# Optimization experiments

Hardware: AMD Instinct MI355X
Metric: run time of the kernel (lower is better)

The kernel has to match this reference:

```python
import jax, jax.numpy as jnp
import numpy as np

EPS_SINK = 0.05
MAX_ITER = 50
THRESH = 0.1
LN_EPS = 1e-5


def _nu_from_score_map(score_map):
    # score_map: [B, K, H, W] -> nu: [B, K]
    B, K, H, W = score_map.shape
    pred = jnp.argmax(score_map, axis=1).reshape(B, H * W)      # [B, HW]
    one_hot = jax.nn.one_hot(pred, K, dtype=score_map.dtype)     # [B, HW, K]
    counts = one_hot.sum(axis=1)                                 # [B, K]
    nu = counts / (counts.sum(axis=1, keepdims=True) + 1e-8)
    nu = nu + 1e-6
    return nu / nu.sum(axis=1, keepdims=True)


def _sinkhorn(x, y, nu):
    # x: [B, N, C], y: [B, M, C], nu: [B, M]
    B, N, _ = x.shape
    M = y.shape[1]
    xn = x / jnp.linalg.norm(x, axis=2, keepdims=True)
    yn = y / jnp.linalg.norm(y, axis=2, keepdims=True)
    cost = 1.0 - jnp.einsum('bnc,bmc->bnm', xn, yn)              # [B, N, M]
    Kmat = jnp.exp(-cost / EPS_SINK)
    mu = jnp.full((B, N), 1.0 / N, dtype=x.dtype)
    u0 = jnp.zeros((B, N), dtype=x.dtype)
    v0 = jnp.zeros((B, M), dtype=x.dtype)

    def step(carry, _):
        u, v, done = carry
        u_new = mu / (jnp.einsum('bnm,bm->bn', Kmat, v) + 1e-8)
        v_new = nu / (jnp.einsum('bnm,bn->bm', Kmat, u_new) + 1e-8)
        err = jnp.abs(u_new - u).sum(-1).mean()
        # torch breaks AFTER the update, so the breaking iteration's u,v are kept;
        # 'done' freezes subsequent iterations (early-stop semantics).
        u_out = jnp.where(done, u, u_new)
        v_out = jnp.where(done, v, v_new)
        return (u_out, v_out, done | (err < THRESH)), None

    (u, v, _), _ = jax.lax.scan(step, (u0, v0, jnp.array(False)), None, length=MAX_ITER)
    pi = u[:, :, None] * Kmat * v[:, None, :]                    # [B, N, M]
    ot_cost = jnp.sum(pi * cost, axis=(1, 2))                    # [B] (reduction='none')
    return ot_cost, pi


def _layernorm(x, gamma, beta):
    mean = x.mean(-1, keepdims=True)
    var = ((x - mean) ** 2).mean(-1, keepdims=True)
    return (x - mean) * jax.lax.rsqrt(var + LN_EPS) * gamma + beta


def setup_inputs() -> dict:
    key = jax.random.key(0)
    k1, k2, k3, k4 = jax.random.split(key, 4)
    B, HW, C, K, H, W = 16, 4096, 512, 32, 64, 64
    return {
        'source_feat': jax.random.normal(k1, (B, HW, C), jnp.float32),
        'target_feat_matrix': jax.random.normal(k2, (B, K, C), jnp.float32),
        'score_map': jax.random.normal(k3, (B, K, H, W), jnp.float32),
        'fusion_w': jax.random.normal(k4, (2 * C, C), jnp.float32) * (1.0 / np.sqrt(2 * C)),
        'fusion_b': jnp.zeros((C,), jnp.float32),
        'ln_gamma': jnp.ones((C,), jnp.float32),
        'ln_beta': jnp.zeros((C,), jnp.float32),
    }


def reference(source_feat, target_feat_matrix, score_map, fusion_w, fusion_b, ln_gamma, ln_beta):
    nu = _nu_from_score_map(score_map)
    ot_loss, pi = _sinkhorn(source_feat, target_feat_matrix, nu)
    pi_norm = pi / (pi.sum(axis=2, keepdims=True) + 1e-8)
    aligned = jnp.einsum('bnm,bmc->bnc', pi_norm, target_feat_matrix)
    fused_in = jnp.concatenate([source_feat, aligned], axis=-1)   # [B, N, 2C]
    out = _layernorm(fused_in @ fusion_w + fusion_b, ln_gamma, ln_beta)
    return out, ot_loss, pi
```

## Files before the change

kernel.cpp:

```cpp
#include <hip/hip_runtime.h>
#include <hip/hip_bf16.h>

typedef __attribute__((ext_vector_type(8))) short bf16x8;
typedef __attribute__((ext_vector_type(4))) float f32x4;
typedef __attribute__((ext_vector_type(8))) unsigned short us8;

#define MFMA16(a, b, c) __builtin_amdgcn_mfma_f32_16x16x32_bf16((a), (b), (c), 0, 0, 0)

static constexpr int Bn = 16;
static constexpr int Nn = 4096;
static constexpr int Cn = 512;
static constexpr int Mn = 32;
static constexpr int NR = Bn * Nn;

static constexpr size_t OFF_XBF  = 0;
static constexpr size_t OFF_XINV = 67108864;
static constexpr size_t OFF_YN   = OFF_XINV + 262144;
static constexpr size_t OFF_YR   = OFF_YN + 524288;
static constexpr size_t OFF_WT   = OFF_YR + 524288;
static constexpr size_t OFF_ZT   = OFF_WT + 1048576;
static constexpr size_t OFF_CNT  = OFF_ZT + 524288;
static constexpr size_t OFF_VERR = OFF_CNT + 2048;
static constexpr size_t OFF_JS   = OFF_VERR + 3200;
static constexpr size_t OFF_VTR  = OFF_JS + 256;
static constexpr size_t OFF_K    = OFF_VTR + 102400;
static constexpr size_t OFF_PIN  = OFF_K + 8388608;

__device__ __forceinline__ unsigned short f2bf(float f) {
  union { float f; unsigned u; } x; x.f = f;
  return (unsigned short)((x.u + 0x7FFFu + ((x.u >> 16) & 1u)) >> 16);
}
__device__ __forceinline__ float bf2f(unsigned short h) {
  union { unsigned u; float f; } x; x.u = ((unsigned)h) << 16;
  return x.f;
}
__device__ __forceinline__ float bflo(unsigned u) {
  union { unsigned v; float f; } x; x.v = u << 16; return x.f;
}
__device__ __forceinline__ float bfhi(unsigned u) {
  union { unsigned v; float f; } x; x.v = u & 0xFFFF0000u; return x.f;
}

__global__ void k_init(int* __restrict__ cnts, float* __restrict__ ot, int* __restrict__ gflag) {
  int t = threadIdx.x;
  if (t < 512) cnts[t] = 0;
  if (t < 16) ot[t] = 0.f;
  if (t < 32) gflag[t] = 0;
}

__global__ __launch_bounds__(256) void k_xprep(const float* __restrict__ x,
                                               unsigned short* __restrict__ xbf,
                                               float* __restrict__ xinv) {
  int wid = threadIdx.x >> 6, l = threadIdx.x & 63;
  int row = blockIdx.x * 4 + wid;
  const float4* p = (const float4*)(x + (size_t)row * Cn);
  float4 a0 = p[l];
  float4 a1 = p[64 + l];
  float s = a0.x*a0.x + a0.y*a0.y + a0.z*a0.z + a0.w*a0.w
          + a1.x*a1.x + a1.y*a1.y + a1.z*a1.z + a1.w*a1.w;
  #pragma unroll
  for (int d = 1; d < 64; d <<= 1) s += __shfl_xor(s, d, 64);
  ushort4 o0, o1;
  o0.x = f2bf(a0.x); o0.y = f2bf(a0.y); o0.z = f2bf(a0.z); o0.w = f2bf(a0.w);
  o1.x = f2bf(a1.x); o1.y = f2bf(a1.y); o1.z = f2bf(a1.z); o1.w = f2bf(a1.w);
  ushort4* q = (ushort4*)(xbf + (size_t)row * Cn);
  q[l] = o0; q[64 + l] = o1;
  if (l == 0) xinv[row] = rsqrtf(s);
}

__global__ __launch_bounds__(256) void k_ynorm(const float* __restrict__ y,
                                               unsigned short* __restrict__ ynbf,
                                               unsigned short* __restrict__ yrbf) {
  int wid = threadIdx.x >> 6, l = threadIdx.x & 63;
  int row = blockIdx.x * 4 + wid;
  const float4* p = (const float4*)(y + (size_t)row * Cn);
  float4 a0 = p[l];
  float4 a1 = p[64 + l];
  float s = a0.x*a0.x + a0.y*a0.y + a0.z*a0.z + a0.w*a0.w
          + a1.x*a1.x + a1.y*a1.y + a1.z*a1.z + a1.w*a1.w;
  #pragma unroll
  for (int d = 1; d < 64; d <<= 1) s += __shfl_xor(s, d, 64);
  float inv = rsqrtf(s);
  ushort4 r0, r1, n0, n1;
  r0.x = f2bf(a0.x); r0.y = f2bf(a0.y); r0.z = f2bf(a0.z); r0.w = f2bf(a0.w);
  r1.x = f2bf(a1.x); r1.y = f2bf(a1.y); r1.z = f2bf(a1.z); r1.w = f2bf(a1.w);
  n0.x = f2bf(a0.x*inv); n0.y = f2bf(a0.y*inv); n0.z = f2bf(a0.z*inv); n0.w = f2bf(a0.w*inv);
  n1.x = f2bf(a1.x*inv); n1.y = f2bf(a1.y*inv); n1.z = f2bf(a1.z*inv); n1.w = f2bf(a1.w*inv);
  ushort4* qr = (ushort4*)(yrbf + (size_t)row * Cn);
  ushort4* qn = (ushort4*)(ynbf + (size_t)row * Cn);
  qr[l] = r0; qr[64 + l] = r1;
  qn[l] = n0; qn[64 + l] = n1;
}

__global__ __launch_bounds__(256) void k_nu(const float* __restrict__ sm, int* __restrict__ cnts) {
  int g = blockIdx.x * 256 + threadIdx.x;
  int b = g >> 12, p = g & 4095;
  const float* base = sm + (size_t)b * Mn * Nn;
  float best = base[p];
  int bi = 0;
  #pragma unroll 4
  for (int k = 1; k < Mn; k++) {
    float v = base[(size_t)k * Nn + p];
    if (v > best) { best = v; bi = k; }
  }
  __shared__ int lc[Mn];
  if (threadIdx.x < Mn) lc[threadIdx.x] = 0;
  __syncthreads();
  atomicAdd(&lc[bi], 1);
  __syncthreads();
  if (threadIdx.x < Mn) atomicAdd(&cnts[b * Mn + threadIdx.x], lc[threadIdx.x]);
}

__global__ __launch_bounds__(256) void k_wt(const float* __restrict__ w, unsigned short* __restrict__ wt) {
  __shared__ float tile[32][33];
  int k0 = blockIdx.x * 32;
  int n0 = blockIdx.y * 32;
  int tx = threadIdx.x & 31, ty = threadIdx.x >> 5;
  #pragma unroll
  for (int i = 0; i < 4; i++) tile[ty + 8*i][tx] = w[(size_t)(k0 + ty + 8*i) * 512 + n0 + tx];
  __syncthreads();
  #pragma unroll
  for (int i = 0; i < 4; i++)
    wt[(size_t)(n0 + ty + 8*i) * 1024 + k0 + tx] = f2bf(tile[tx][ty + 8*i]);
}

__global__ __launch_bounds__(256) void k_zt(const unsigned short* __restrict__ yraw,
                                            const unsigned short* __restrict__ wt,
                                            unsigned short* __restrict__ zt) {
  int wv = blockIdx.x * 4 + (threadIdx.x >> 6);
  int l = threadIdx.x & 63;
  int b = wv >> 6, rem = wv & 63, mt = rem >> 5, nt = rem & 31;
  int kg = l >> 4;
  const unsigned short* ap = yraw + ((size_t)(b * 32 + mt * 16 + (l & 15)) * 512 + kg * 8);
  const unsigned short* bp = wt + ((size_t)(nt * 16 + (l & 15)) * 1024 + 512 + kg * 8);
  f32x4 acc = {0.f, 0.f, 0.f, 0.f};
  #pragma unroll
  for (int ks = 0; ks < 16; ks++) {
    bf16x8 a = *(const bf16x8*)(ap + ks * 32);
    bf16x8 bb = *(const bf16x8*)(bp + ks * 32);
    acc = MFMA16(a, bb, acc);
  }
  int n = nt * 16 + (l & 15);
  #pragma unroll
  for (int r = 0; r < 4; r++) {
    int m = mt * 16 + kg * 4 + r;
    zt[((size_t)b * 512 + n) * 32 + m] = f2bf(acc[r]);
  }
}

__global__ __launch_bounds__(256) void k_cost(const unsigned short* __restrict__ xbf,
                                              const float* __restrict__ xinv,
                                              const unsigned short* __restrict__ ynbf,
                                              float* __restrict__ kmat) {
  int wv = blockIdx.x * 4 + (threadIdx.x >> 6);
  int l = threadIdx.x & 63;
  int r0 = wv * 16;
  int b = r0 >> 12;
  int kg = l >> 4;
  const unsigned short* ap = xbf + ((size_t)(r0 + (l & 15)) * 512 + kg * 8);
  const unsigned short* b0p = ynbf + ((size_t)(b * 32 + (l & 15)) * 512 + kg * 8);
  const unsigned short* b1p = ynbf + ((size_t)(b * 32 + 16 + (l & 15)) * 512 + kg * 8);
  f32x4 acc0 = {0.f, 0.f, 0.f, 0.f}, acc1 = {0.f, 0.f, 0.f, 0.f};
  #pragma unroll
  for (int ks = 0; ks < 16; ks++) {
    bf16x8 a = *(const bf16x8*)(ap + ks * 32);
    acc0 = MFMA16(a, *(const bf16x8*)(b0p + ks * 32), acc0);
    acc1 = MFMA16(a, *(const bf16x8*)(b1p + ks * 32), acc1);
  }
  int col = l & 15;
  #pragma unroll
  for (int r = 0; r < 4; r++) {
    int row = r0 + kg * 4 + r;
    float inv = xinv[row];
    kmat[(size_t)row * 32 + col]      = __expf(-20.f * (1.f - acc0[r] * inv));
    kmat[(size_t)row * 32 + col + 16] = __expf(-20.f * (1.f - acc1[r] * inv));
  }
}

__global__ __launch_bounds__(512, 2) void k_sink1(const float* __restrict__ kmat,
                                                  const int* __restrict__ cnts,
                                                  float* __restrict__ verr,
                                                  float* __restrict__ vtrace,
                                                  int* __restrict__ gflag,
                                                  float* __restrict__ gpart) {
  int bid = blockIdx.x;
  int h = bid >> 4;
  int b = bid & 15;
  int self = bid;
  int peer = (bid + 16) & 31;
  int t = threadIdx.x;
  int lane = t & 63;
  int w = t >> 6;
  __shared__ float v_s[32], nu_s[32];
  __shared__ float red_s[8];
  __shared__ float cred[8][32];
  __shared__ float vhist[50][32];
  __shared__ float ehist[50];
  __shared__ float errtot_s;
  if (t < 32) {
    float c = (float)cnts[b * 32 + t];
    float nu = c / (4096.f + 1e-8f) + 1e-6f;
    float ss = nu;
    #pragma unroll
    for (int d = 1; d < 32; d <<= 1) ss += __shfl_xor(ss, d, 64);
    nu_s[t] = nu / ss;
    v_s[t] = 0.f;
  }
  unsigned kq[64];
  {
    const float4* kp = (const float4*)(kmat + ((size_t)b * 4096 + h * 2048 + (size_t)t * 4) * 32);
    #pragma unroll
    for (int r = 0; r < 4; r++) {
      #pragma unroll
      for (int q = 0; q < 8; q++) {
        float4 kv = kp[r * 8 + q];
        kq[r * 16 + q * 2]     = (unsigned)f2bf(kv.x) | ((unsigned)f2bf(kv.y) << 16);
        kq[r * 16 + q * 2 + 1] = (unsigned)f2bf(kv.z) | ((unsigned)f2bf(kv.w) << 16);
      }
    }
  }
  float uprev[4] = {0.f, 0.f, 0.f, 0.f};
  __syncthreads();

  for (int iter = 0; iter < 50; iter++) {
    float accA[4] = {0.f, 0.f, 0.f, 0.f}, accB[4] = {0.f, 0.f, 0.f, 0.f};
    {
      const float4* v4 = (const float4*)v_s;
      #pragma unroll
      for (int j = 0; j < 8; j++) {
        float4 vv = v4[j];
        #pragma unroll
        for (int hh = 0; hh < 2; hh++) {
          int q = j * 2 + hh;
          float va = hh ? vv.z : vv.x;
          float vb = hh ? vv.w : vv.y;
          #pragma unroll
          for (int r = 0; r < 4; r++) {
            unsigned pk = kq[r * 16 + q];
            accA[r] += bflo(pk) * va;
            accB[r] += bfhi(pk) * vb;
          }
        }
      }
    }
    float un[4];
    float errloc = 0.f;
    #pragma unroll
    for (int r = 0; r < 4; r++) {
      un[r] = (1.0f/4096.f) / (accA[r] + accB[r] + 1e-8f);
      errloc += fabsf(un[r] - uprev[r]);
      uprev[r] = un[r];
    }
    #pragma unroll
    for (int d = 1; d < 64; d <<= 1) errloc += __shfl_xor(errloc, d, 64);
    if (lane == 0) red_s[w] = errloc;

    #define FOLD(MASK, HALF)                                        \
    {                                                               \
      bool up_ = (lane & (MASK)) != 0;                              \
      _Pragma("unroll")                                             \
      for (int i = 0; i < (HALF); i++) {                            \
        float s_ = up_ ? cacc[i] : cacc[i + (HALF)];                \
        float r_ = __shfl_xor(s_, (MASK), 64);                      \
        cacc[i] = (up_ ? cacc[i + (HALF)] : cacc[i]) + r_;          \
      }                                                             \
    }
    #pragma unroll
    for (int ch = 0; ch < 2; ch++) {
      float cacc[16];
      #pragma unroll
      for (int c = 0; c < 16; c++) cacc[c] = 0.f;
      #pragma unroll
      for (int qq = 0; qq < 8; qq++) {
        int q = ch * 8 + qq;
        #pragma unroll
        for (int r = 0; r < 4; r++) {
          unsigned pk = kq[r * 16 + q];
          cacc[2*qq]   += bflo(pk) * un[r];
          cacc[2*qq+1] += bfhi(pk) * un[r];
        }
      }
      FOLD(1, 8)
      FOLD(2, 4)
      FOLD(4, 2)
      FOLD(8, 1)
      cacc[0] += __shfl_xor(cacc[0], 16, 64);
      cacc[0] += __shfl_xor(cacc[0], 32, 64);
      int col4 = ((lane & 1) << 3) | ((lane & 2) << 1) | ((lane & 4) >> 1) | ((lane & 8) >> 3);
      if (lane < 16) cred[w][ch * 16 + col4] = cacc[0];
    }
    #undef FOLD
    __syncthreads();

    if (w == 0) {
      float sumP = 0.f, errP = 0.f;
      if (lane < 32) {
        #pragma unroll
        for (int ww = 0; ww < 8; ww++) sumP += cred[ww][lane];
      }
      if (lane == 0) {
        #pragma unroll
        for (int ww = 0; ww < 8; ww++) errP += red_s[ww];
      }
      int slotS = ((self << 1) | (iter & 1)) * 33;
      int slotP = ((peer << 1) | (iter & 1)) * 33;
      if (lane < 32)
        __hip_atomic_store(&gpart[slotS + lane], sumP, __ATOMIC_RELAXED, __HIP_MEMORY_SCOPE_AGENT);
      if (lane == 0) {
        __hip_atomic_store(&gpart[slotS + 32], errP, __ATOMIC_RELAXED, __HIP_MEMORY_SCOPE_AGENT);
        __hip_atomic_store(&gflag[self], iter + 1, __ATOMIC_RELEASE, __HIP_MEMORY_SCOPE_AGENT);
        while (__hip_atomic_load(&gflag[peer], __ATOMIC_ACQUIRE, __HIP_MEMORY_SCOPE_AGENT) < iter + 1)
          __builtin_amdgcn_s_sleep(1);
      }
      float part = 0.f, perr = 0.f;
      if (lane < 32)
        part = __hip_atomic_load(&gpart[slotP + lane], __ATOMIC_RELAXED, __HIP_MEMORY_SCOPE_AGENT);
      if (lane == 0)
        perr = __hip_atomic_load(&gpart[slotP + 32], __ATOMIC_RELAXED, __HIP_MEMORY_SCOPE_AGENT);
      float etot = __shfl(errP + perr, 0, 64);
      if (lane < 32) {
        float v = nu_s[lane] / (sumP + part + 1e-8f);
        v_s[lane] = v;
        if (h == 0) vhist[iter][lane] = v;
      }
      if (lane == 0) {
        errtot_s = etot;
        if (h == 0) ehist[iter] = etot;
      }
    }
    __syncthreads();
    if (errtot_s == 0.0f) {
      if (h == 0 && t < 32) {
        float vv = v_s[t];
        for (int k = iter; k < 50; k++) vhist[k][t] = vv;
        if (t == 0) for (int k = iter; k < 50; k++) ehist[k] = 0.f;
      }
      break;
    }
  }

  if (h == 0) {
    __syncthreads();
    for (int idx = t; idx < 1600; idx += 512) {
      int k = idx >> 5, m = idx & 31;
      vtrace[k * 512 + b * 32 + m] = vhist[k][m];
    }
    if (t < 50) verr[t * 16 + b] = ehist[t];
  }
}

__global__ void k_stop(const float* __restrict__ verr, int* __restrict__ jstar) {
  int t = threadIdx.x;
  float m = 1e30f;
  if (t < 50) {
    float s = 0.f;
    #pragma unroll
    for (int b2 = 0; b2 < 16; b2++) s += verr[t * 16 + b2];
    m = s * (1.f / 16.f);
  }
  unsigned long long mask = __ballot(m < 0.1f);
  if (t == 0) *jstar = mask ? (int)(__ffsll(mask) - 1) : 49;
}

__global__ __launch_bounds__(256) void k_pi(const float* __restrict__ kmat,
                                            const float* __restrict__ vtrace,
                                            const int* __restrict__ jstar,
                                            unsigned short* __restrict__ pinbf,
                                            float* __restrict__ piout,
                                            float* __restrict__ otout) {
  int gr = blockIdx.x * 256 + threadIdx.x;
  int b = gr >> 12;
  __shared__ float vp_s[32], vc_s[32];
  __shared__ float red[4];
  if (threadIdx.x < 32) {
    int j = *jstar;
    vp_s[threadIdx.x] = (j == 0) ? 0.f : vtrace[(j - 1) * 512 + b * 32 + threadIdx.x];
    vc_s[threadIdx.x] = vtrace[j * 512 + b * 32 + threadIdx.x];
  }
  __syncthreads();
  const float4* kp = (const float4*)(kmat + (size_t)gr * 32);
  float4 K4[8];
  #pragma unroll
  for (int q = 0; q < 8; q++) K4[q] = kp[q];
  float qd = 0.f;
  #pragma unroll
  for (int q = 0; q < 8; q++)
    qd += K4[q].x * vp_s[q*4] + K4[q].y * vp_s[q*4+1] + K4[q].z * vp_s[q*4+2] + K4[q].w * vp_s[q*4+3];
  float u = (1.0f/4096.f) / (qd + 1e-8f);
  float pi[32];
  float s = 0.f, ot = 0.f;
  #pragma unroll
  for (int q = 0; q < 8; q++) {
    float kv[4] = {K4[q].x, K4[q].y, K4[q].z, K4[q].w};
    #pragma unroll
    for (int r = 0; r < 4; r++) {
      int m = q * 4 + r;
      float p = u * kv[r] * vc_s[m];
      pi[m] = p;
      s += p;
      ot += p * (-0.05f * __logf(kv[r]));
    }
  }
  float inv = 1.0f / (s + 1e-8f);
  float4* po = (float4*)(piout + (size_t)gr * 32);
  #pragma unroll
  for (int q = 0; q < 8; q++) {
    float4 w; w.x = pi[q*4]; w.y = pi[q*4+1]; w.z = pi[q*4+2]; w.w = pi[q*4+3];
    po[q] = w;
  }
  us8* pb = (us8*)(pinbf + (size_t)gr * 32);
  #pragma unroll
  for (int q = 0; q < 4; q++) {
    us8 v8;
    #pragma unroll
    for (int r = 0; r < 8; r++) v8[r] = f2bf(pi[q*8+r] * inv);
    pb[q] = v8;
  }
  #pragma unroll
  for (int d = 1; d < 64; d <<= 1) ot += __shfl_xor(ot, d, 64);
  if ((threadIdx.x & 63) == 0) red[threadIdx.x >> 6] = ot;
  __syncthreads();
  if (threadIdx.x == 0) atomicAdd(&otout[b], red[0] + red[1] + red[2] + red[3]);
}

__global__ __launch_bounds__(256, 2) void k_fusion(const unsigned short* __restrict__ xbf,
                                                   const unsigned short* __restrict__ pinbf,
                                                   const unsigned short* __restrict__ wt,
                                                   const unsigned short* __restrict__ zt,
                                                   const float* __restrict__ bias,
                                                   const float* __restrict__ gamma,
                                                   const float* __restrict__ beta_,
                                                   float* __restrict__ out) {
  int t = threadIdx.x;
  int wid = t >> 6, l = t & 63;
  int row0 = blockIdx.x * 64;
  int b = row0 >> 12;
  int col0 = wid * 128;
  int m16 = l & 15, kg = l >> 4;
  f32x4 acc[4][8];
  #pragma unroll
  for (int rt = 0; rt < 4; rt++)
    #pragma unroll
    for (int ct = 0; ct < 8; ct++) acc[rt][ct] = (f32x4){0.f, 0.f, 0.f, 0.f};

  const unsigned short* aB[4];
  const unsigned short* bB[8];
  #pragma unroll
  for (int rt = 0; rt < 4; rt++) aB[rt] = xbf + ((size_t)(row0 + rt * 16 + m16) * 512 + kg * 8);
  #pragma unroll
  for (int ct = 0; ct < 8; ct++) bB[ct] = wt + ((size_t)(col0 + ct * 16 + m16) * 1024 + kg * 8);

  for (int ks = 0; ks < 16; ks++) {
    bf16x8 A[4], Bf[8];
    #pragma unroll
    for (int rt = 0; rt < 4; rt++) A[rt] = *(const bf16x8*)(aB[rt] + ks * 32);
    #pragma unroll
    for (int ct = 0; ct < 8; ct++) Bf[ct] = *(const bf16x8*)(bB[ct] + ks * 32);
    #pragma unroll
    for (int rt = 0; rt < 4; rt++)
      #pragma unroll
      for (int ct = 0; ct < 8; ct++) acc[rt][ct] = MFMA16(A[rt], Bf[ct], acc[rt][ct]);
  }
  {
    bf16x8 A[4], Bf[8];
    #pragma unroll
    for (int rt = 0; rt < 4; rt++)
      A[rt] = *(const bf16x8*)(pinbf + (size_t)(row0 + rt * 16 + m16) * 32 + kg * 8);
    #pragma unroll
    for (int ct = 0; ct < 8; ct++)
      Bf[ct] = *(const bf16x8*)(zt + ((size_t)(b * 512 + col0 + ct * 16 + m16)) * 32 + kg * 8);
    #pragma unroll
    for (int rt = 0; rt < 4; rt++)
      #pragma unroll
      for (int ct = 0; ct < 8; ct++) acc[rt][ct] = MFMA16(A[rt], Bf[ct], acc[rt][ct]);
  }
  float bi[8], ga[8], be[8];
  #pragma unroll
  for (int ct = 0; ct < 8; ct++) {
    int c = col0 + ct * 16 + m16;
    bi[ct] = bias[c]; ga[ct] = gamma[c]; be[ct] = beta_[c];
  }
  __shared__ float p1[4][64], p2[4][64];
  #pragma unroll
  for (int rt = 0; rt < 4; rt++) {
    #pragma unroll
    for (int r = 0; r < 4; r++) {
      float s1 = 0.f, s2 = 0.f;
      #pragma unroll
      for (int ct = 0; ct < 8; ct++) {
        float val = acc[rt][ct][r] + bi[ct];
        s1 += val; s2 += val * val;
      }
      #pragma unroll
      for (int d = 1; d < 16; d <<= 1) {
        s1 += __shfl_xor(s1, d, 64);
        s2 += __shfl_xor(s2, d, 64);
      }
      if (m16 == 0) {
        int rloc = rt * 16 + kg * 4 + r;
        p1[wid][rloc] = s1; p2[wid][rloc] = s2;
      }
    }
  }
  __syncthreads();
  __shared__ float lnM[64], lnR[64];
  if (t < 64) {
    float s1 = p1[0][t] + p1[1][t] + p1[2][t] + p1[3][t];
    float s2 = p2[0][t] + p2[1][t] + p2[2][t] + p2[3][t];
    float mean = s1 * (1.f / 512.f);
    float var = s2 * (1.f / 512.f) - mean * mean;
    lnM[t] = mean;
    lnR[t] = rsqrtf(var + 1e-5f);
  }
  __syncthreads();
  #pragma unroll
  for (int rt = 0; rt < 4; rt++) {
    #pragma unroll
    for (int r = 0; r < 4; r++) {
      int rloc = rt * 16 + kg * 4 + r;
      float mean = lnM[rloc], rst = lnR[rloc];
      #pragma unroll
      for (int ct = 0; ct < 8; ct++) {
        float val = acc[rt][ct][r] + bi[ct];
        out[(size_t)(row0 + rloc) * 512 + col0 + ct * 16 + m16] = (val - mean) * rst * ga[ct] + be[ct];
      }
    }
  }
}

extern "C" void kernel_launch(void* const* d_in, const int* in_sizes, int n_in,
                              void* d_out, int out_size, void* d_ws, size_t ws_size,
                              hipStream_t stream) {
  const float* x  = (const float*)d_in[0];
  const float* y  = (const float*)d_in[1];
  const float* sm = (const float*)d_in[2];
  const float* fw = (const float*)d_in[3];
  const float* fb = (const float*)d_in[4];
  const float* g  = (const float*)d_in[5];
  const float* be = (const float*)d_in[6];

  char* ws = (char*)d_ws;
  unsigned short* xbf   = (unsigned short*)(ws + OFF_XBF);
  float*          xinv  = (float*)(ws + OFF_XINV);
  unsigned short* ynbf  = (unsigned short*)(ws + OFF_YN);
  unsigned short* yrbf  = (unsigned short*)(ws + OFF_YR);
  unsigned short* wtbf  = (unsigned short*)(ws + OFF_WT);
  unsigned short* ztbf  = (unsigned short*)(ws + OFF_ZT);
  int*            cnts  = (int*)(ws + OFF_CNT);
  float*          verr  = (float*)(ws + OFF_VERR);
  int*            jst   = (int*)(ws + OFF_JS);
  float*          vtr   = (float*)(ws + OFF_VTR);
  float*          kmat  = (float*)(ws + OFF_K);
  unsigned short* pinbf = (unsigned short*)(ws + OFF_PIN);
  int*            gflag = (int*)(ws + OFF_PIN);
  float*          gpart = (float*)(ws + OFF_PIN + 128);

  float* outp = (float*)d_out;
  float* otp  = outp + (size_t)Bn * Nn * Cn;
  float* pip  = otp + Bn;

  hipLaunchKernelGGL(k_init, dim3(1), dim3(512), 0, stream, cnts, otp, gflag);
  hipLaunchKernelGGL(k_xprep, dim3(NR / 4), dim3(256), 0, stream, x, xbf, xinv);
  hipLaunchKernelGGL(k_ynorm, dim3(128), dim3(256), 0, stream, y, ynbf, yrbf);
  hipLaunchKernelGGL(k_nu, dim3(256), dim3(256), 0, stream, sm, cnts);
  hipLaunchKernelGGL(k_wt, dim3(32, 16), dim3(256), 0, stream, fw, wtbf);
  hipLaunchKernelGGL(k_zt, dim3(256), dim3(256), 0, stream, yrbf, wtbf, ztbf);
  hipLaunchKernelGGL(k_cost, dim3(1024), dim3(256), 0, stream, xbf, xinv, ynbf, kmat);
  hipLaunchKernelGGL(k_sink1, dim3(32), dim3(512), 0, stream, kmat, cnts, verr, vtr, gflag, gpart);
  hipLaunchKernelGGL(k_stop, dim3(1), dim3(64), 0, stream, verr, jst);
  hipLaunchKernelGGL(k_pi, dim3(256), dim3(256), 0, stream, kmat, vtr, jst, pinbf, pip, otp);
  hipLaunchKernelGGL(k_fusion, dim3(1024), dim3(256), 0, stream,
                     xbf, pinbf, wtbf, ztbf, fb, g, be, outp);
}
```

Before: 618.8 us.

## Run Sinkhorn per batch in one 1024-thread block, dropping cross-block spin sync

The Sinkhorn iteration kernel used two 512-thread blocks per batch that exchanged partial column sums and error values each iteration through global atomics and a spin-wait flag. It now uses a single 1024-thread block per batch, so the reduction stays in shared memory and the global handshake, the flag initialisation and the partial buffers are removed. In exchange, only 16 blocks run instead of 32, which halves the number of CUs working on the latency-bound loop, and the larger block may face tighter register limits for the 64-register K cache.

Result: slower. 904.1 us (+46.1%).

```diff
diff --git a/kernel.cpp b/kernel.cpp
--- a/kernel.cpp
+++ b/kernel.cpp
@@ -41,11 +41,10 @@
   union { unsigned v; float f; } x; x.v = u & 0xFFFF0000u; return x.f;
 }
 
-__global__ void k_init(int* __restrict__ cnts, float* __restrict__ ot, int* __restrict__ gflag) {
+__global__ void k_init(int* __restrict__ cnts, float* __restrict__ ot) {
   int t = threadIdx.x;
   if (t < 512) cnts[t] = 0;
   if (t < 16) ot[t] = 0.f;
-  if (t < 32) gflag[t] = 0;
 }
 
 __global__ __launch_bounds__(256) void k_xprep(const float* __restrict__ x,
@@ -177,23 +176,17 @@
   }
 }
 
-__global__ __launch_bounds__(512, 2) void k_sink1(const float* __restrict__ kmat,
-                                                  const int* __restrict__ cnts,
-                                                  float* __restrict__ verr,
-                                                  float* __restrict__ vtrace,
-                                                  int* __restrict__ gflag,
-                                                  float* __restrict__ gpart) {
-  int bid = blockIdx.x;
-  int h = bid >> 4;
-  int b = bid & 15;
-  int self = bid;
-  int peer = (bid + 16) & 31;
+__global__ __launch_bounds__(1024, 4) void k_sink1(const float* __restrict__ kmat,
+                                                   const int* __restrict__ cnts,
+                                                   float* __restrict__ verr,
+                                                   float* __restrict__ vtrace) {
+  int b = blockIdx.x;
   int t = threadIdx.x;
   int lane = t & 63;
   int w = t >> 6;
   __shared__ float v_s[32], nu_s[32];
-  __shared__ float red_s[8];
-  __shared__ float cred[8][32];
+  __shared__ float red_s[16];
+  __shared__ float cred[16][32];
   __shared__ float vhist[50][32];
   __shared__ float ehist[50];
   __shared__ float errtot_s;
@@ -208,7 +201,7 @@
   }
   unsigned kq[64];
   {
-    const float4* kp = (const float4*)(kmat + ((size_t)b * 4096 + h * 2048 + (size_t)t * 4) * 32);
+    const float4* kp = (const float4*)(kmat + ((size_t)b * 4096 + (size_t)t * 4) * 32);
     #pragma unroll
     for (int r = 0; r < 4; r++) {
       #pragma unroll
@@ -296,41 +289,23 @@
       float sumP = 0.f, errP = 0.f;
       if (lane < 32) {
         #pragma unroll
-        for (int ww = 0; ww < 8; ww++) sumP += cred[ww][lane];
+        for (int ww = 0; ww < 16; ww++) sumP += cred[ww][lane];
       }
       if (lane == 0) {
         #pragma unroll
-        for (int ww = 0; ww < 8; ww++) errP += red_s[ww];
-      }
-      int slotS = ((self << 1) | (iter & 1)) * 33;
-      int slotP = ((peer << 1) | (iter & 1)) * 33;
-      if (lane < 32)
-        __hip_atomic_store(&gpart[slotS + lane], sumP, __ATOMIC_RELAXED, __HIP_MEMORY_SCOPE_AGENT);
-      if (lane == 0) {
-        __hip_atomic_store(&gpart[slotS + 32], errP, __ATOMIC_RELAXED, __HIP_MEMORY_SCOPE_AGENT);
-        __hip_atomic_store(&gflag[self], iter + 1, __ATOMIC_RELEASE, __HIP_MEMORY_SCOPE_AGENT);
-        while (__hip_atomic_load(&gflag[peer], __ATOMIC_ACQUIRE, __HIP_MEMORY_SCOPE_AGENT) < iter + 1)
-          __builtin_amdgcn_s_sleep(1);
-      }
-      float part = 0.f, perr = 0.f;
-      if (lane < 32)
-        part = __hip_atomic_load(&gpart[slotP + lane], __ATOMIC_RELAXED, __HIP_MEMORY_SCOPE_AGENT);
-      if (lane == 0)
-        perr = __hip_atomic_load(&gpart[slotP + 32], __ATOMIC_RELAXED, __HIP_MEMORY_SCOPE_AGENT);
-      float etot = __shfl(errP + perr, 0, 64);
+        for (int ww = 0; ww < 16; ww++) errP += red_s[ww];
+        errtot_s = errP;
+        ehist[iter] = errP;
+      }
       if (lane < 32) {
-        float v = nu_s[lane] / (sumP + part + 1e-8f);
+        float v = nu_s[lane] / (sumP + 1e-8f);
         v_s[lane] = v;
-        if (h == 0) vhist[iter][lane] = v;
-      }
-      if (lane == 0) {
-        errtot_s = etot;
-        if (h == 0) ehist[iter] = etot;
+        vhist[iter][lane] = v;
       }
     }
     __syncthreads();
     if (errtot_s == 0.0f) {
-      if (h == 0 && t < 32) {
+      if (t < 32) {
         float vv = v_s[t];
         for (int k = iter; k < 50; k++) vhist[k][t] = vv;
         if (t == 0) for (int k = iter; k < 50; k++) ehist[k] = 0.f;
@@ -339,14 +314,12 @@
     }
   }
 
-  if (h == 0) {
-    __syncthreads();
-    for (int idx = t; idx < 1600; idx += 512) {
-      int k = idx >> 5, m = idx & 31;
-      vtrace[k * 512 + b * 32 + m] = vhist[k][m];
-    }
-    if (t < 50) verr[t * 16 + b] = ehist[t];
-  }
+  __syncthreads();
+  for (int idx = t; idx < 1600; idx += 1024) {
+    int k = idx >> 5, m = idx & 31;
+    vtrace[k * 512 + b * 32 + m] = vhist[k][m];
+  }
+  if (t < 50) verr[t * 16 + b] = ehist[t];
 }
 
 __global__ void k_stop(const float* __restrict__ verr, int* __restrict__ jstar) {
@@ -552,21 +525,19 @@
   float*          vtr   = (float*)(ws + OFF_VTR);
   float*          kmat  = (float*)(ws + OFF_K);
   unsigned short* pinbf = (unsigned short*)(ws + OFF_PIN);
-  int*            gflag = (int*)(ws + OFF_PIN);
-  float*          gpart = (float*)(ws + OFF_PIN + 128);
 
   float* outp = (float*)d_out;
   float* otp  = outp + (size_t)Bn * Nn * Cn;
   float* pip  = otp + Bn;
 
-  hipLaunchKernelGGL(k_init, dim3(1), dim3(512), 0, stream, cnts, otp, gflag);
+  hipLaunchKernelGGL(k_init, dim3(1), dim3(512), 0, stream, cnts, otp);
   hipLaunchKernelGGL(k_xprep, dim3(NR / 4), dim3(256), 0, stream, x, xbf, xinv);
   hipLaunchKernelGGL(k_ynorm, dim3(128), dim3(256), 0, stream, y, ynbf, yrbf);
   hipLaunchKernelGGL(k_nu, dim3(256), dim3(256), 0, stream, sm, cnts);
   hipLaunchKernelGGL(k_wt, dim3(32, 16), dim3(256), 0, stream, fw, wtbf);
   hipLaunchKernelGGL(k_zt, dim3(256), dim3(256), 0, stream, yrbf, wtbf, ztbf);
   hipLaunchKernelGGL(k_cost, dim3(1024), dim3(256), 0, stream, xbf, xinv, ynbf, kmat);
-  hipLaunchKernelGGL(k_sink1, dim3(32), dim3(512), 0, stream, kmat, cnts, verr, vtr, gflag, gpart);
+  hipLaunchKernelGGL(k_sink1, dim3(16), dim3(1024), 0, stream, kmat, cnts, verr, vtr);
   hipLaunchKernelGGL(k_stop, dim3(1), dim3(64), 0, stream, verr, jst);
   hipLaunchKernelGGL(k_pi, dim3(256), dim3(256), 0, stream, kmat, vtr, jst, pinbf, pip, otp);
   hipLaunchKernelGGL(k_fusion, dim3(1024), dim3(256), 0, stream,
```
